# Kernel tuning notes

Hardware: AMD Instinct MI355X
Metric: run time of the kernel (lower is better)

## Reference

```python
import jax, jax.numpy as jnp
import numpy as np

DELTA = 0.2
TOPK = 10
RECALL_KS = (1, 5, 10)


def setup_inputs() -> dict:
    key = jax.random.key(0)
    k1, k2 = jax.random.split(key)
    B, D = 8192, 256
    x = jax.random.normal(k1, (B, D), dtype=jnp.float32)
    y = jax.random.normal(k2, (B, D), dtype=jnp.float32)
    return {"x": x, "y": y}


def reference(x, y):
    B = x.shape[0]
    # L2-normalize rows (matches x / sqrt(sum(x*x), keepdim))
    xn = x / jnp.sqrt(jnp.sum(x * x, axis=1, keepdims=True))
    yn = y / jnp.sqrt(jnp.sum(y * y, axis=1, keepdims=True))
    sim = xn @ yn.T                      # [B, B]
    diag = jnp.diagonal(sim)             # [B]
    cor = diag[:, None]                  # cor_similarity[i, j] = sim[i, i]
    loss_mat = jnp.maximum(0.0, sim - cor + DELTA) + jnp.maximum(0.0, sim.T - cor + DELTA)
    # zero the diagonal (vectorized version of the python loop)
    loss_mat = loss_mat * (1.0 - jnp.eye(B, dtype=loss_mat.dtype))
    loss = jnp.sum(loss_mat) / B

    # metrics (no grad in original)
    score = sim - cor                    # [B, B]
    _, pred = jax.lax.top_k(score, TOPK)  # [B, 10] indices, descending
    # torch code: pred.t() [10,B] eq arange(B); equivalent untransposed:
    correct = pred == jnp.arange(B)[:, None]          # [B, 10]
    correct_per_rank = jnp.sum(correct, axis=0)        # [10] hits at rank j
    recall = jnp.stack([jnp.sum(correct[:, :k]) for k in RECALL_KS]).astype(jnp.int32)
    # ndcg weight ln(2)/ln(2+j) for rank j (0-based), matching math.log(2)/math.log(2+j)
    w = jnp.log(2.0) / jnp.log(2.0 + jnp.arange(TOPK, dtype=jnp.float32))
    ndcg = jnp.stack([jnp.sum(correct_per_rank[:k].astype(jnp.float32) * w[:k]) for k in RECALL_KS])
    return loss, recall, ndcg
```

## Files before the change

### kernel.cpp

```cpp
#include <hip/hip_runtime.h>
#include <math.h>

#define NB 8192
#define ND 256
#define DELTA_F 0.2f
#define NT 24

typedef __attribute__((ext_vector_type(8))) __bf16 bf16x8;
typedef __attribute__((ext_vector_type(4))) __bf16 bf16x4;
typedef __attribute__((ext_vector_type(4))) float f32x4;

__device__ __forceinline__ void gload16(const void* g, void* l) {
  __builtin_amdgcn_global_load_lds(
      (const __attribute__((address_space(1))) void*)g,
      (__attribute__((address_space(3))) void*)l, 16, 0, 0);
}

__global__ __launch_bounds__(256) void normalize_split_k(
    const float* __restrict__ x, const float* __restrict__ y,
    __bf16* __restrict__ Xh, __bf16* __restrict__ Xl,
    __bf16* __restrict__ Yh, __bf16* __restrict__ Yl,
    float* __restrict__ dd, float* __restrict__ loss_accum, int* __restrict__ cnt) {
  const int w = threadIdx.x >> 6, lane = threadIdx.x & 63;
  const int i = blockIdx.x * 4 + w;
  const size_t rbase = (size_t)i * ND;
  const float4 xv = *(const float4*)&x[rbase + lane * 4];
  const float4 yv = *(const float4*)&y[rbase + lane * 4];
  float sxx = xv.x * xv.x + xv.y * xv.y + xv.z * xv.z + xv.w * xv.w;
  float syy = yv.x * yv.x + yv.y * yv.y + yv.z * yv.z + yv.w * yv.w;
  float sxy = xv.x * yv.x + xv.y * yv.y + xv.z * yv.z + xv.w * yv.w;
#pragma unroll
  for (int o = 1; o < 64; o <<= 1) {
    sxx += __shfl_xor(sxx, o, 64);
    syy += __shfl_xor(syy, o, 64);
    sxy += __shfl_xor(sxy, o, 64);
  }
  const float ix = 1.0f / sqrtf(sxx);
  const float iy = 1.0f / sqrtf(syy);
  if (lane == 0) {
    dd[i] = sxy * ix * iy;
    cnt[i] = 0;
    if (i == 0) loss_accum[0] = 0.0f;
  }
  const float xs[4] = {xv.x * ix, xv.y * ix, xv.z * ix, xv.w * ix};
  const float ys[4] = {yv.x * iy, yv.y * iy, yv.z * iy, yv.w * iy};
  bf16x4 xh, xl, yh, yl;
#pragma unroll
  for (int e = 0; e < 4; ++e) {
    const __bf16 h = (__bf16)xs[e];
    xh[e] = h; xl[e] = (__bf16)(xs[e] - (float)h);
    const __bf16 g = (__bf16)ys[e];
    yh[e] = g; yl[e] = (__bf16)(ys[e] - (float)g);
  }
  *(bf16x4*)&Xh[rbase + lane * 4] = xh;
  *(bf16x4*)&Xl[rbase + lane * 4] = xl;
  *(bf16x4*)&Yh[rbase + lane * 4] = yh;
  *(bf16x4*)&Yl[rbase + lane * 4] = yl;
}

__global__ __launch_bounds__(512, 2) void gemm_mfma(
    const __bf16* __restrict__ Xh, const __bf16* __restrict__ Xl,
    const __bf16* __restrict__ Yh, const __bf16* __restrict__ Yl,
    const float* __restrict__ dd,
    float* __restrict__ loss_accum, int* __restrict__ cnt) {
  __shared__ __bf16 sAB[4][2][256][32];
  __shared__ int c_loc[256];
  __shared__ float lred[8];

  const int tid = threadIdx.x;
  const int bid = blockIdx.x;
  const int xcd = bid & 7, idx = bid >> 3;
  const int bi = xcd * 4 + (idx & 3);
  const int bj = (idx >> 5) * 8 + ((idx >> 2) & 7);
  const int row0 = bi * 256, col0 = bj * 256;

  const int lane = tid & 63, wid = tid >> 6;
  const int wr = wid >> 2, wc = wid & 3;
  const int lr = lane & 15, lkc = lane >> 4;

  if (tid < 256) c_loc[tid] = 0;

  const int rowl = tid >> 2;
  const int swz = (tid & 3) ^ ((tid >> 3) & 3);
  const size_t offA0 = (size_t)(row0 + rowl) * (ND * 2) + swz * 16;
  const size_t offB0 = (size_t)(col0 + rowl) * (ND * 2) + swz * 16;
  char* const lds0 = (char*)&sAB[0][0][0][0];

  f32x4 acc[8][4];
#pragma unroll
  for (int m = 0; m < 8; ++m)
#pragma unroll
    for (int n = 0; n < 4; ++n) acc[m][n] = (f32x4)(0.0f);

  auto stage = [&](int t) {
    const char* pa = (const char*)((t >= 8 && t < 16) ? Xl : Xh) + (t & 7) * 64;
    const char* pb = (const char*)((t >= 16) ? Yl : Yh) + (t & 7) * 64;
    char* lb = lds0 + (t & 3) * 32768;
    gload16(pa + offA0,         lb + tid * 16);
    gload16(pa + offA0 + 65536, lb + 8192 + tid * 16);
    gload16(pb + offB0,         lb + 16384 + tid * 16);
    gload16(pb + offB0 + 65536, lb + 24576 + tid * 16);
  };

  const int cko = (lkc ^ ((lr >> 1) & 3)) * 8;
  const int arow = wr * 128 + lr;
  const int brow = wc * 64 + lr;

#pragma unroll
  for (int t = 0; t < 3; ++t) stage(t);

#pragma unroll
  for (int t = 0; t < NT; ++t) {
    if (t + 3 < NT) stage(t + 3);
    __builtin_amdgcn_sched_barrier(0);
    if (t < NT - 3)       asm volatile("s_waitcnt vmcnt(12)\n\ts_barrier" ::: "memory");
    else if (t == NT - 3) asm volatile("s_waitcnt vmcnt(8)\n\ts_barrier" ::: "memory");
    else if (t == NT - 2) asm volatile("s_waitcnt vmcnt(4)\n\ts_barrier" ::: "memory");
    else                  asm volatile("s_waitcnt vmcnt(0)\n\ts_barrier" ::: "memory");

    const int b = t & 3;
    bf16x8 bf[4], af[8];
#pragma unroll
    for (int n = 0; n < 4; ++n) bf[n] = *(const bf16x8*)&sAB[b][1][brow + n * 16][cko];
#pragma unroll
    for (int m = 0; m < 8; ++m) af[m] = *(const bf16x8*)&sAB[b][0][arow + m * 16][cko];

    __builtin_amdgcn_s_setprio(1);
#pragma unroll
    for (int m = 0; m < 4; ++m)
#pragma unroll
      for (int n = 0; n < 4; ++n)
        acc[m][n] = __builtin_amdgcn_mfma_f32_16x16x32_bf16(af[m], bf[n], acc[m][n], 0, 0, 0);
    __builtin_amdgcn_s_setprio(0);
    asm volatile("s_barrier" ::: "memory");
    __builtin_amdgcn_s_setprio(1);
#pragma unroll
    for (int m = 4; m < 8; ++m)
#pragma unroll
      for (int n = 0; n < 4; ++n)
        acc[m][n] = __builtin_amdgcn_mfma_f32_16x16x32_bf16(af[m], bf[n], acc[m][n], 0, 0, 0);
    __builtin_amdgcn_s_setprio(0);
    asm volatile("s_barrier" ::: "memory");
  }

  float djv[4];
#pragma unroll
  for (int n = 0; n < 4; ++n) djv[n] = dd[col0 + wc * 64 + n * 16 + lr];

  float lsum = 0.f;
#pragma unroll
  for (int m = 0; m < 8; ++m) {
    const int rbase = wr * 128 + m * 16 + lkc * 4;
#pragma unroll
    for (int q = 0; q < 4; ++q) {
      const int gi = row0 + rbase + q;
      const float dival = dd[gi];
      int cl = 0;
#pragma unroll
      for (int n = 0; n < 4; ++n) {
        const int gj = col0 + wc * 64 + n * 16 + lr;
        const float s = acc[m][n][q];
        if (gi != gj) {
          lsum += fmaxf(0.f, s - dival + DELTA_F) + fmaxf(0.f, s - djv[n] + DELTA_F);
          cl += (s > dival) ? 1 : 0;
        }
      }
      cl += __shfl_xor(cl, 1, 64);
      cl += __shfl_xor(cl, 2, 64);
      cl += __shfl_xor(cl, 4, 64);
      cl += __shfl_xor(cl, 8, 64);
      if (lr == 0) atomicAdd(&c_loc[rbase + q], cl);
    }
  }

#pragma unroll
  for (int o = 32; o > 0; o >>= 1) lsum += __shfl_down(lsum, o, 64);
  if (lane == 0) lred[wid] = lsum;
  __syncthreads();
  if (tid == 0) {
    float s = 0.f;
#pragma unroll
    for (int w = 0; w < 8; ++w) s += lred[w];
    atomicAdd(loss_accum, s);
  }
  if (tid < 256) atomicAdd(&cnt[row0 + tid], c_loc[tid]);
}

__global__ __launch_bounds__(256) void finalize_k(
    const float* __restrict__ loss_accum, const int* __restrict__ cnt,
    float* __restrict__ out) {
  const int t = threadIdx.x;
  float a6[6] = {0.f, 0.f, 0.f, 0.f, 0.f, 0.f};
  for (int i = t; i < NB; i += 256) {
    const int c = cnt[i];
    if (c < 10) {
      const float w = 0.69314718055994531f / logf(2.0f + (float)c);
      a6[2] += 1.f; a6[5] += w;
      if (c < 5) { a6[1] += 1.f; a6[4] += w; }
      if (c < 1) { a6[0] += 1.f; a6[3] += w; }
    }
  }
  __shared__ float red[6][4];
#pragma unroll
  for (int j = 0; j < 6; ++j) {
    float v = a6[j];
#pragma unroll
    for (int o = 32; o > 0; o >>= 1) v += __shfl_down(v, o, 64);
    if ((t & 63) == 0) red[j][t >> 6] = v;
  }
  __syncthreads();
  if (t == 0) {
    out[0] = loss_accum[0] / (float)NB;
#pragma unroll
    for (int j = 0; j < 6; ++j)
      out[1 + j] = red[j][0] + red[j][1] + red[j][2] + red[j][3];
  }
}

extern "C" void kernel_launch(void* const* d_in, const int* in_sizes, int n_in,
                              void* d_out, int out_size, void* d_ws, size_t ws_size,
                              hipStream_t stream) {
  const float* x = (const float*)d_in[0];
  const float* y = (const float*)d_in[1];
  float* out = (float*)d_out;

  char* ws = (char*)d_ws;
  float* loss_accum = (float*)ws;
  int* cnt = (int*)(ws + 256);
  float* dd = (float*)(ws + 256 + 32768);

  const size_t splitOff = 256 + 2 * 32768;
  const size_t matB = (size_t)NB * ND * 2;
  __bf16* Xh = (__bf16*)(ws + splitOff);
  __bf16* Xl = (__bf16*)(ws + splitOff + matB);
  __bf16* Yh = (__bf16*)(ws + splitOff + 2 * matB);
  __bf16* Yl = (__bf16*)(ws + splitOff + 3 * matB);

  hipLaunchKernelGGL(normalize_split_k, dim3(NB / 4), dim3(256), 0, stream,
                     x, y, Xh, Xl, Yh, Yl, dd, loss_accum, cnt);
  hipLaunchKernelGGL(gemm_mfma, dim3(1024), dim3(512), 0, stream,
                     Xh, Xl, Yh, Yl, dd, loss_accum, cnt);
  hipLaunchKernelGGL(finalize_k, dim3(1), dim3(256), 0, stream, loss_accum, cnt, out);
}
```

Baseline: 168.2 us.

## Fuse split-bf16 passes into one K loop reusing hi/lo tiles

The GEMM used to stream the three split-precision products (hi·hi, lo·hi, hi·lo) as 24 separate stages. It now runs 8 K-steps, and each step stages all four hi/lo tiles of A and B into a double-buffered LDS region, then issues the three MFMAs per accumulator back to back. This is meant to avoid loading and LDS-reading the hi tiles twice and to drop the intermediate barriers. In exchange, prefetch depth falls from three stages ahead to one. The next stage is also issued before the barrier that protects the buffer other waves may still be reading, which risks a race and exposed load latency.

```diff
diff --git a/kernel.cpp b/kernel.cpp
--- a/kernel.cpp
+++ b/kernel.cpp
@@ -4,7 +4,6 @@
 #define NB 8192
 #define ND 256
 #define DELTA_F 0.2f
-#define NT 24
 
 typedef __attribute__((ext_vector_type(8))) __bf16 bf16x8;
 typedef __attribute__((ext_vector_type(4))) __bf16 bf16x4;
@@ -63,7 +62,7 @@
     const __bf16* __restrict__ Yh, const __bf16* __restrict__ Yl,
     const float* __restrict__ dd,
     float* __restrict__ loss_accum, int* __restrict__ cnt) {
-  __shared__ __bf16 sAB[4][2][256][32];
+  __shared__ __bf16 sAB[2][4][256][32];
   __shared__ int c_loc[256];
   __shared__ float lred[8];
 
@@ -82,8 +81,10 @@
 
   const int rowl = tid >> 2;
   const int swz = (tid & 3) ^ ((tid >> 3) & 3);
-  const size_t offA0 = (size_t)(row0 + rowl) * (ND * 2) + swz * 16;
-  const size_t offB0 = (size_t)(col0 + rowl) * (ND * 2) + swz * 16;
+  const char* const pAh = (const char*)Xh + (size_t)(row0 + rowl) * 512 + swz * 16;
+  const char* const pAl = (const char*)Xl + (size_t)(row0 + rowl) * 512 + swz * 16;
+  const char* const pBh = (const char*)Yh + (size_t)(col0 + rowl) * 512 + swz * 16;
+  const char* const pBl = (const char*)Yl + (size_t)(col0 + rowl) * 512 + swz * 16;
   char* const lds0 = (char*)&sAB[0][0][0][0];
 
   f32x4 acc[8][4];
@@ -93,54 +94,56 @@
     for (int n = 0; n < 4; ++n) acc[m][n] = (f32x4)(0.0f);
 
   auto stage = [&](int t) {
-    const char* pa = (const char*)((t >= 8 && t < 16) ? Xl : Xh) + (t & 7) * 64;
-    const char* pb = (const char*)((t >= 16) ? Yl : Yh) + (t & 7) * 64;
-    char* lb = lds0 + (t & 3) * 32768;
-    gload16(pa + offA0,         lb + tid * 16);
-    gload16(pa + offA0 + 65536, lb + 8192 + tid * 16);
-    gload16(pb + offB0,         lb + 16384 + tid * 16);
-    gload16(pb + offB0 + 65536, lb + 24576 + tid * 16);
+    char* lb = lds0 + (t & 1) * 65536;
+    const int ko = t * 64;
+    gload16(pAh + ko,         lb + tid * 16);
+    gload16(pAh + ko + 65536, lb +  8192 + tid * 16);
+    gload16(pAl + ko,         lb + 16384 + tid * 16);
+    gload16(pAl + ko + 65536, lb + 24576 + tid * 16);
+    gload16(pBh + ko,         lb + 32768 + tid * 16);
+    gload16(pBh + ko + 65536, lb + 40960 + tid * 16);
+    gload16(pBl + ko,         lb + 49152 + tid * 16);
+    gload16(pBl + ko + 65536, lb + 57344 + tid * 16);
   };
 
   const int cko = (lkc ^ ((lr >> 1) & 3)) * 8;
-  const int arow = wr * 128 + lr;
-  const int brow = wc * 64 + lr;
-
-#pragma unroll
-  for (int t = 0; t < 3; ++t) stage(t);
-
-#pragma unroll
-  for (int t = 0; t < NT; ++t) {
-    if (t + 3 < NT) stage(t + 3);
-    __builtin_amdgcn_sched_barrier(0);
-    if (t < NT - 3)       asm volatile("s_waitcnt vmcnt(12)\n\ts_barrier" ::: "memory");
-    else if (t == NT - 3) asm volatile("s_waitcnt vmcnt(8)\n\ts_barrier" ::: "memory");
-    else if (t == NT - 2) asm volatile("s_waitcnt vmcnt(4)\n\ts_barrier" ::: "memory");
-    else                  asm volatile("s_waitcnt vmcnt(0)\n\ts_barrier" ::: "memory");
-
-    const int b = t & 3;
-    bf16x8 bf[4], af[8];
-#pragma unroll
-    for (int n = 0; n < 4; ++n) bf[n] = *(const bf16x8*)&sAB[b][1][brow + n * 16][cko];
-#pragma unroll
-    for (int m = 0; m < 8; ++m) af[m] = *(const bf16x8*)&sAB[b][0][arow + m * 16][cko];
-
-    __builtin_amdgcn_s_setprio(1);
-#pragma unroll
-    for (int m = 0; m < 4; ++m)
-#pragma unroll
-      for (int n = 0; n < 4; ++n)
-        acc[m][n] = __builtin_amdgcn_mfma_f32_16x16x32_bf16(af[m], bf[n], acc[m][n], 0, 0, 0);
-    __builtin_amdgcn_s_setprio(0);
-    asm volatile("s_barrier" ::: "memory");
-    __builtin_amdgcn_s_setprio(1);
-#pragma unroll
-    for (int m = 4; m < 8; ++m)
-#pragma unroll
-      for (int n = 0; n < 4; ++n)
-        acc[m][n] = __builtin_amdgcn_mfma_f32_16x16x32_bf16(af[m], bf[n], acc[m][n], 0, 0, 0);
-    __builtin_amdgcn_s_setprio(0);
-    asm volatile("s_barrier" ::: "memory");
+
+  stage(0);
+#pragma unroll
+  for (int t = 0; t < 8; ++t) {
+    if (t < 7) stage(t + 1);
+    if (t < 7) asm volatile("s_waitcnt vmcnt(8)\n\ts_barrier" ::: "memory");
+    else       asm volatile("s_waitcnt vmcnt(0)\n\ts_barrier" ::: "memory");
+
+    const int b = t & 1;
+    bf16x8 bh4[4], bl4[4];
+#pragma unroll
+    for (int n = 0; n < 4; ++n) {
+      bh4[n] = *(const bf16x8*)&sAB[b][2][wc * 64 + n * 16 + lr][cko];
+      bl4[n] = *(const bf16x8*)&sAB[b][3][wc * 64 + n * 16 + lr][cko];
+    }
+#pragma unroll
+    for (int half = 0; half < 2; ++half) {
+      bf16x8 ah4[4], al4[4];
+#pragma unroll
+      for (int m = 0; m < 4; ++m) {
+        const int r = wr * 128 + (half * 4 + m) * 16 + lr;
+        ah4[m] = *(const bf16x8*)&sAB[b][0][r][cko];
+        al4[m] = *(const bf16x8*)&sAB[b][1][r][cko];
+      }
+      __builtin_amdgcn_s_setprio(1);
+#pragma unroll
+      for (int m = 0; m < 4; ++m)
+#pragma unroll
+        for (int n = 0; n < 4; ++n) {
+          f32x4 a = acc[half * 4 + m][n];
+          a = __builtin_amdgcn_mfma_f32_16x16x32_bf16(ah4[m], bh4[n], a, 0, 0, 0);
+          a = __builtin_amdgcn_mfma_f32_16x16x32_bf16(ah4[m], bl4[n], a, 0, 0, 0);
+          a = __builtin_amdgcn_mfma_f32_16x16x32_bf16(al4[m], bh4[n], a, 0, 0, 0);
+          acc[half * 4 + m][n] = a;
+        }
+      __builtin_amdgcn_s_setprio(0);
+    }
   }
 
   float djv[4];
```

Result: faster. 139.7 us, median of 2 (-16.9%).

## Restructure GEMM main loop into double-buffered two-k-step stages with interleaved loads

Applied to the files above, without the earlier changes.

Replaces the 4-deep single-k-step LDS ring with a 2-slot double buffer where each iteration covers two 32-wide k-steps. The next stage's global-to-LDS loads are split into four chunks interleaved with four MFMA phases, with A fragments for later phases read before the barrier. This aims to cut barrier count per k and overlap LDS reads and global loads with MFMA. In exchange it has a shallower prefetch depth and more fragment registers live.

```diff
diff --git a/kernel.cpp b/kernel.cpp
--- a/kernel.cpp
+++ b/kernel.cpp
@@ -4,7 +4,6 @@
 #define NB 8192
 #define ND 256
 #define DELTA_F 0.2f
-#define NT 24
 
 typedef __attribute__((ext_vector_type(8))) __bf16 bf16x8;
 typedef __attribute__((ext_vector_type(4))) __bf16 bf16x4;
@@ -63,7 +62,7 @@
     const __bf16* __restrict__ Yh, const __bf16* __restrict__ Yl,
     const float* __restrict__ dd,
     float* __restrict__ loss_accum, int* __restrict__ cnt) {
-  __shared__ __bf16 sAB[4][2][256][32];
+  __shared__ __bf16 sAB[2][2][2][256][32];
   __shared__ int c_loc[256];
   __shared__ float lred[8];
 
@@ -82,9 +81,8 @@
 
   const int rowl = tid >> 2;
   const int swz = (tid & 3) ^ ((tid >> 3) & 3);
-  const size_t offA0 = (size_t)(row0 + rowl) * (ND * 2) + swz * 16;
-  const size_t offB0 = (size_t)(col0 + rowl) * (ND * 2) + swz * 16;
-  char* const lds0 = (char*)&sAB[0][0][0][0];
+  const size_t offA = (size_t)(row0 + rowl) * 512 + swz * 16;
+  const size_t offB = (size_t)(col0 + rowl) * 512 + swz * 16;
 
   f32x4 acc[8][4];
 #pragma unroll
@@ -92,55 +90,71 @@
 #pragma unroll
     for (int n = 0; n < 4; ++n) acc[m][n] = (f32x4)(0.0f);
 
-  auto stage = [&](int t) {
-    const char* pa = (const char*)((t >= 8 && t < 16) ? Xl : Xh) + (t & 7) * 64;
-    const char* pb = (const char*)((t >= 16) ? Yl : Yh) + (t & 7) * 64;
-    char* lb = lds0 + (t & 3) * 32768;
-    gload16(pa + offA0,         lb + tid * 16);
-    gload16(pa + offA0 + 65536, lb + 8192 + tid * 16);
-    gload16(pb + offB0,         lb + 16384 + tid * 16);
-    gload16(pb + offB0 + 65536, lb + 24576 + tid * 16);
+  auto stage_chunk = [&](int it, int q) {
+    const int t = 2 * it + (q >> 1);
+    const int term = t >> 3;
+    const int kb = (t & 7) * 64;
+    char* lb = (char*)&sAB[it & 1][q >> 1][q & 1][0][0];
+    const char* src;
+    if ((q & 1) == 0)
+      src = (const char*)(term == 1 ? Xl : Xh) + offA + kb;
+    else
+      src = (const char*)(term == 2 ? Yl : Yh) + offB + kb;
+    gload16(src, lb + tid * 16);
+    gload16(src + 65536, lb + 8192 + tid * 16);
   };
 
   const int cko = (lkc ^ ((lr >> 1) & 3)) * 8;
-  const int arow = wr * 128 + lr;
-  const int brow = wc * 64 + lr;
-
-#pragma unroll
-  for (int t = 0; t < 3; ++t) stage(t);
-
-#pragma unroll
-  for (int t = 0; t < NT; ++t) {
-    if (t + 3 < NT) stage(t + 3);
-    __builtin_amdgcn_sched_barrier(0);
-    if (t < NT - 3)       asm volatile("s_waitcnt vmcnt(12)\n\ts_barrier" ::: "memory");
-    else if (t == NT - 3) asm volatile("s_waitcnt vmcnt(8)\n\ts_barrier" ::: "memory");
-    else if (t == NT - 2) asm volatile("s_waitcnt vmcnt(4)\n\ts_barrier" ::: "memory");
-    else                  asm volatile("s_waitcnt vmcnt(0)\n\ts_barrier" ::: "memory");
-
-    const int b = t & 3;
-    bf16x8 bf[4], af[8];
-#pragma unroll
-    for (int n = 0; n < 4; ++n) bf[n] = *(const bf16x8*)&sAB[b][1][brow + n * 16][cko];
-#pragma unroll
-    for (int m = 0; m < 8; ++m) af[m] = *(const bf16x8*)&sAB[b][0][arow + m * 16][cko];
-
-    __builtin_amdgcn_s_setprio(1);
-#pragma unroll
-    for (int m = 0; m < 4; ++m)
-#pragma unroll
-      for (int n = 0; n < 4; ++n)
-        acc[m][n] = __builtin_amdgcn_mfma_f32_16x16x32_bf16(af[m], bf[n], acc[m][n], 0, 0, 0);
-    __builtin_amdgcn_s_setprio(0);
-    asm volatile("s_barrier" ::: "memory");
-    __builtin_amdgcn_s_setprio(1);
-#pragma unroll
-    for (int m = 4; m < 8; ++m)
-#pragma unroll
-      for (int n = 0; n < 4; ++n)
-        acc[m][n] = __builtin_amdgcn_mfma_f32_16x16x32_bf16(af[m], bf[n], acc[m][n], 0, 0, 0);
-    __builtin_amdgcn_s_setprio(0);
-    asm volatile("s_barrier" ::: "memory");
+
+#pragma unroll
+  for (int q = 0; q < 4; ++q) stage_chunk(0, q);
+
+#pragma unroll
+  for (int it = 0; it < 12; ++it) {
+    const int s = it & 1;
+    bf16x8 bfr[4][2];
+#pragma unroll
+    for (int p = 0; p < 4; ++p) {
+      bf16x8 afr[2][2];
+      if (p > 0) {
+#pragma unroll
+        for (int m = 0; m < 2; ++m)
+#pragma unroll
+          for (int ks = 0; ks < 2; ++ks)
+            afr[m][ks] = *(const bf16x8*)&sAB[s][ks][0][wr * 128 + (p * 2 + m) * 16 + lr][cko];
+      }
+      if (it < 11) stage_chunk(it + 1, p);
+      if (p == 0) {
+        if (it < 11) asm volatile("s_waitcnt vmcnt(2)" ::: "memory");
+        else         asm volatile("s_waitcnt vmcnt(0)" ::: "memory");
+      }
+      asm volatile("s_barrier" ::: "memory");
+      if (p == 0) {
+#pragma unroll
+        for (int n = 0; n < 4; ++n)
+#pragma unroll
+          for (int ks = 0; ks < 2; ++ks)
+            bfr[n][ks] = *(const bf16x8*)&sAB[s][ks][1][wc * 64 + n * 16 + lr][cko];
+#pragma unroll
+        for (int m = 0; m < 2; ++m)
+#pragma unroll
+          for (int ks = 0; ks < 2; ++ks)
+            afr[m][ks] = *(const bf16x8*)&sAB[s][ks][0][wr * 128 + m * 16 + lr][cko];
+      }
+      asm volatile("s_waitcnt lgkmcnt(0)" ::: "memory");
+      __builtin_amdgcn_sched_barrier(0);
+      __builtin_amdgcn_s_setprio(1);
+#pragma unroll
+      for (int ks = 0; ks < 2; ++ks)
+#pragma unroll
+        for (int m = 0; m < 2; ++m)
+#pragma unroll
+          for (int n = 0; n < 4; ++n)
+            acc[p * 2 + m][n] = __builtin_amdgcn_mfma_f32_16x16x32_bf16(
+                afr[m][ks], bfr[n][ks], acc[p * 2 + m][n], 0, 0, 0);
+      __builtin_amdgcn_s_setprio(0);
+      asm volatile("s_barrier" ::: "memory");
+    }
   }
 
   float djv[4];
```

Result: slower. 185.7 us (+10.4%).
